# Kernel tuning notes

Hardware: AMD Instinct MI355X
Metric: run time of the kernel (lower is better)

The kernel has to match this reference:

```python
import jax, jax.numpy as jnp
import numpy as np

# Model dims (match init_kwargs)
B, L, DH = 4, 1024, 2048
D = 128          # head_dim
HQ, HK, HV = 16, 4, 4
H = 16           # expanded_num_heads = max(HQ, HK, HV)
K = 4            # short conv kernel size
EPS = 1e-5


def causal_depthwise_conv_silu(x, w):
    """ShortConvolution: causal depthwise conv1d + SiLU. x: [B,L,C], w: [C,K]."""
    Lx = x.shape[1]
    xp = jnp.pad(x, ((0, 0), (K - 1, 0), (0, 0)))
    y = sum(xp[:, j:j + Lx] * w[:, j] for j in range(K))
    return jax.nn.silu(y)


def _l2norm(t):
    return t * jax.lax.rsqrt(jnp.sum(t * t, axis=-1, keepdims=True) + 1e-6)


def setup_inputs() -> dict:
    key = jax.random.key(0)
    ks = jax.random.split(key, 14)
    s = 0.02
    # dt_bias init per module: dt ~ logspace(1e-3, 1e-1), inv softplus
    u = jax.random.uniform(ks[7], (H,))
    dt = jnp.exp(u * (np.log(0.1) - np.log(0.001)) + np.log(0.001))
    dt = jnp.clip(dt, 1e-4)
    dt_bias = dt + jnp.log(-jnp.expm1(-dt))
    return {
        "hidden_states": jax.random.normal(ks[0], (B, L, DH), jnp.float32),
        "Wq": jax.random.normal(ks[1], (DH, HQ * D), jnp.float32) * s,
        "Wk": jax.random.normal(ks[2], (DH, HK * D), jnp.float32) * s,
        "Wv": jax.random.normal(ks[3], (DH, HV * D), jnp.float32) * s,
        "Wb": jax.random.normal(ks[4], (DH, H), jnp.float32) * s,
        "Wgk": jax.random.normal(ks[5], (DH, H), jnp.float32) * s,
        "A_log": jnp.log(jax.random.uniform(ks[6], (H,), minval=1e-3, maxval=16.0)),
        "dt_bias": dt_bias,
        "conv_q": jax.random.normal(ks[8], (HQ * D, K), jnp.float32) * 0.1,
        "conv_k": jax.random.normal(ks[9], (HK * D, K), jnp.float32) * 0.1,
        "conv_v": jax.random.normal(ks[10], (HV * D, K), jnp.float32) * 0.1,
        "Wg": jax.random.normal(ks[11], (DH, H * D), jnp.float32) * s,
        "o_norm_w": jnp.ones((D,), jnp.float32),
        "Wo": jax.random.normal(ks[12], (H * D, DH), jnp.float32) * s,
    }


def reference(hidden_states, Wq, Wk, Wv, Wb, Wgk, A_log, dt_bias,
              conv_q, conv_k, conv_v, Wg, o_norm_w, Wo):
    x = hidden_states                                   # [B,L,DH]
    # projections + short causal conv + silu
    q = causal_depthwise_conv_silu(x @ Wq, conv_q).reshape(B, L, HQ, D)
    k = causal_depthwise_conv_silu(x @ Wk, conv_k).reshape(B, L, HK, D)
    v = causal_depthwise_conv_silu(x @ Wv, conv_v).reshape(B, L, HV, D)
    # GQA expansion: '... h d -> ... (h g) d' == repeat each head g times
    k = jnp.repeat(k, H // HK, axis=2)                  # [B,L,H,D]
    v = jnp.repeat(v, H // HV, axis=2)
    # gating scalars
    beta = jax.nn.sigmoid(x @ Wb)                       # [B,L,H]
    g = -jnp.exp(A_log) * jax.nn.softplus(x @ Wgk + dt_bias)  # [B,L,H] (log decay <= 0)
    # qk l2-norm (as in kernel), q scaled by D**-0.5
    q = _l2norm(q) * (D ** -0.5)
    k = _l2norm(k)
    # gated delta-rule recurrence: S_t = exp(g_t) S_{t-1} + beta_t k_t (v_t - k_t^T exp(g_t) S_{t-1})
    qT = q.transpose(1, 0, 2, 3)                        # [L,B,H,D]
    kT = k.transpose(1, 0, 2, 3)
    vT = v.transpose(1, 0, 2, 3)
    gT = g.transpose(1, 0, 2)                           # [L,B,H]
    bT = beta.transpose(1, 0, 2)

    def step(S, inp):
        q_t, k_t, v_t, g_t, b_t = inp
        S = S * jnp.exp(g_t)[..., None, None]           # decay state [B,H,D,D]
        v_res = v_t - jnp.einsum('bhk,bhkv->bhv', k_t, S)
        S = S + b_t[..., None, None] * (k_t[..., None] * v_res[:, :, None, :])
        o_t = jnp.einsum('bhk,bhkv->bhv', q_t, S)
        return S, o_t

    S0 = jnp.zeros((B, H, D, D), jnp.float32)
    _, oT = jax.lax.scan(step, S0, (qT, kT, vT, gT, bT))
    o = oT.transpose(1, 0, 2, 3)                        # [B,L,H,D]
    # FusedRMSNormGated: rmsnorm(o) * w * silu(gate), then output projection
    gate = (x @ Wg).reshape(B, L, H, D)
    o = o * jax.lax.rsqrt(jnp.mean(o * o, axis=-1, keepdims=True) + EPS)
    o = o * o_norm_w * jax.nn.silu(gate)
    return o.reshape(B, L, H * D) @ Wo                  # [B,L,DH]
```

## Files before the change

kernel.cpp:

```cpp
#include <hip/hip_runtime.h>
#include <hip/hip_bf16.h>
#include <math.h>

#define Bb 4
#define Ls 1024
#define DHc 2048
#define Dh 128
#define HQc 16
#define HKc 4
#define Hc 16
#define Mrows 4096
#define CC 64
#define NCH 16

typedef __attribute__((ext_vector_type(8))) short bf16x8;
typedef __attribute__((ext_vector_type(4))) float f32x4;

__device__ inline unsigned short f2b(float f) {
    __hip_bfloat16 h = __float2bfloat16(f);
    return *(unsigned short*)&h;
}
__device__ inline float b2f(unsigned short u) {
    __hip_bfloat16 h = *(__hip_bfloat16*)&u;
    return __bfloat162float(h);
}
__device__ inline bf16x8 scale_frag(bf16x8 a, float s) {
    union { bf16x8 v; unsigned short u[8]; } x;
    x.v = a;
#pragma unroll
    for (int i = 0; i < 8; i++) x.u[i] = f2b(b2f(x.u[i]) * s);
    return x.v;
}

__device__ inline void load_lds16(const void* g, void* l) {
    __builtin_amdgcn_global_load_lds((const __attribute__((address_space(1))) void*)g,
                                     (__attribute__((address_space(3))) void*)l, 16, 0, 0);
}

__device__ inline void bar_lds() {
    asm volatile("s_waitcnt lgkmcnt(0)" ::: "memory");
    __builtin_amdgcn_s_barrier();
    asm volatile("" ::: "memory");
}

__global__ void f32_to_bf16(const float* __restrict__ in, __hip_bfloat16* __restrict__ out, int n)
{
    int i = (blockIdx.x * 256 + threadIdx.x) * 4;
    if (i >= n) return;
    float4 v = *(const float4*)(in + i);
    __hip_bfloat16 h[4];
    h[0] = __float2bfloat16(v.x); h[1] = __float2bfloat16(v.y);
    h[2] = __float2bfloat16(v.z); h[3] = __float2bfloat16(v.w);
    *(uint2*)(out + i) = *(uint2*)h;
}

__launch_bounds__(256)
__global__ void transpose_to_bf16(const float* __restrict__ W, __hip_bfloat16* __restrict__ BT,
                                  int Krows, int Ncols)
{
    __shared__ float tile[64][65];
    const int n0 = blockIdx.x * 64, k0 = blockIdx.y * 64;
    const int tx = threadIdx.x & 63, ty = threadIdx.x >> 6;
#pragma unroll
    for (int r = ty; r < 64; r += 4)
        tile[r][tx] = W[(size_t)(k0 + r) * Ncols + n0 + tx];
    __syncthreads();
#pragma unroll
    for (int r = ty; r < 64; r += 4)
        BT[(size_t)(n0 + r) * Krows + k0 + tx] = __float2bfloat16(tile[tx][r]);
}

__launch_bounds__(256)
__global__ void gemm_bt_bf16(const __hip_bfloat16* __restrict__ A, const __hip_bfloat16* __restrict__ BT,
                             void* __restrict__ C, int N, int K, int c_bf16)
{
    __shared__ __align__(16) unsigned short As[128 * 32];
    __shared__ __align__(16) unsigned short Bs[128 * 32];
    const int tid = threadIdx.x;
    const int lane = tid & 63;
    const int wave = tid >> 6;
    const int wm = (wave >> 1) * 64, wn = (wave & 1) * 64;
    const int row0 = blockIdx.y * 128, col0 = blockIdx.x * 128;

    const int r0 = (wave * 2 + 0) * 16 + (lane >> 2);
    const int r1 = (wave * 2 + 1) * 16 + (lane >> 2);
    const int kk = ((lane & 3) ^ ((lane >> 3) & 3)) * 8;
    const __hip_bfloat16* Ap0 = A + (size_t)(row0 + r0) * K + kk;
    const __hip_bfloat16* Ap1 = A + (size_t)(row0 + r1) * K + kk;
    const __hip_bfloat16* Bp0 = BT + (size_t)(col0 + r0) * K + kk;
    const __hip_bfloat16* Bp1 = BT + (size_t)(col0 + r1) * K + kk;
    unsigned short* sa0 = &As[(wave * 2 + 0) * 16 * 32];
    unsigned short* sa1 = &As[(wave * 2 + 1) * 16 * 32];
    unsigned short* sb0 = &Bs[(wave * 2 + 0) * 16 * 32];
    unsigned short* sb1 = &Bs[(wave * 2 + 1) * 16 * 32];

    f32x4 acc[4][4];
#pragma unroll
    for (int i = 0; i < 4; i++)
#pragma unroll
        for (int j = 0; j < 4; j++) acc[i][j] = (f32x4){0.f, 0.f, 0.f, 0.f};

    const int fr = lane & 15;
    const int fs = (((lane >> 4) ^ ((fr >> 1) & 3))) * 8;

    for (int k0 = 0; k0 < K; k0 += 32) {
        __syncthreads();
        load_lds16(Ap0, sa0);
        load_lds16(Ap1, sa1);
        load_lds16(Bp0, sb0);
        load_lds16(Bp1, sb1);
        Ap0 += 32; Ap1 += 32; Bp0 += 32; Bp1 += 32;
        __syncthreads();

        bf16x8 af[4], bfr[4];
#pragma unroll
        for (int i = 0; i < 4; i++)
            af[i] = *(const bf16x8*)&As[(wm + i * 16 + fr) * 32 + fs];
#pragma unroll
        for (int j = 0; j < 4; j++)
            bfr[j] = *(const bf16x8*)&Bs[(wn + j * 16 + fr) * 32 + fs];
#pragma unroll
        for (int i = 0; i < 4; i++)
#pragma unroll
            for (int j = 0; j < 4; j++)
                acc[i][j] = __builtin_amdgcn_mfma_f32_16x16x32_bf16(af[i], bfr[j], acc[i][j], 0, 0, 0);
    }

    const int cr = (lane >> 4) * 4;
    const int cc = lane & 15;
#pragma unroll
    for (int i = 0; i < 4; i++)
#pragma unroll
        for (int j = 0; j < 4; j++) {
            size_t base = (size_t)(row0 + wm + i * 16 + cr) * N + (col0 + wn + j * 16 + cc);
#pragma unroll
            for (int p = 0; p < 4; p++) {
                if (c_bf16)
                    ((__hip_bfloat16*)C)[base + (size_t)p * N] = __float2bfloat16(acc[i][j][p]);
                else
                    ((float*)C)[base + (size_t)p * N] = acc[i][j][p];
            }
        }
}

__launch_bounds__(256)
__global__ void gemm_proj_fused(const __hip_bfloat16* __restrict__ A, const __hip_bfloat16* __restrict__ BT,
                                __hip_bfloat16* __restrict__ preQ, __hip_bfloat16* __restrict__ preK,
                                __hip_bfloat16* __restrict__ preV, __hip_bfloat16* __restrict__ gate)
{
    const int K = 2048;
    __shared__ __align__(16) unsigned short As[128 * 32];
    __shared__ __align__(16) unsigned short Bs[128 * 32];
    const int tid = threadIdx.x;
    const int lane = tid & 63;
    const int wave = tid >> 6;
    const int wm = (wave >> 1) * 64, wn = (wave & 1) * 64;
    const int row0 = blockIdx.y * 128;
    const int cb = blockIdx.x;
    const int col0 = cb * 128;

    __hip_bfloat16* Cb; int Nloc, c0loc;
    if (cb < 16)      { Cb = preQ; Nloc = 2048; c0loc = cb * 128; }
    else if (cb < 20) { Cb = preK; Nloc = 512;  c0loc = (cb - 16) * 128; }
    else if (cb < 24) { Cb = preV; Nloc = 512;  c0loc = (cb - 20) * 128; }
    else              { Cb = gate; Nloc = 2048; c0loc = (cb - 24) * 128; }

    const int r0 = (wave * 2 + 0) * 16 + (lane >> 2);
    const int r1 = (wave * 2 + 1) * 16 + (lane >> 2);
    const int kk = ((lane & 3) ^ ((lane >> 3) & 3)) * 8;
    const __hip_bfloat16* Ap0 = A + (size_t)(row0 + r0) * K + kk;
    const __hip_bfloat16* Ap1 = A + (size_t)(row0 + r1) * K + kk;
    const __hip_bfloat16* Bp0 = BT + (size_t)(col0 + r0) * K + kk;
    const __hip_bfloat16* Bp1 = BT + (size_t)(col0 + r1) * K + kk;
    unsigned short* sa0 = &As[(wave * 2 + 0) * 16 * 32];
    unsigned short* sa1 = &As[(wave * 2 + 1) * 16 * 32];
    unsigned short* sb0 = &Bs[(wave * 2 + 0) * 16 * 32];
    unsigned short* sb1 = &Bs[(wave * 2 + 1) * 16 * 32];

    f32x4 acc[4][4];
#pragma unroll
    for (int i = 0; i < 4; i++)
#pragma unroll
        for (int j = 0; j < 4; j++) acc[i][j] = (f32x4){0.f, 0.f, 0.f, 0.f};

    const int fr = lane & 15;
    const int fs = (((lane >> 4) ^ ((fr >> 1) & 3))) * 8;

    for (int k0 = 0; k0 < K; k0 += 32) {
        __syncthreads();
        load_lds16(Ap0, sa0);
        load_lds16(Ap1, sa1);
        load_lds16(Bp0, sb0);
        load_lds16(Bp1, sb1);
        Ap0 += 32; Ap1 += 32; Bp0 += 32; Bp1 += 32;
        __syncthreads();

        bf16x8 af[4], bfr[4];
#pragma unroll
        for (int i = 0; i < 4; i++)
            af[i] = *(const bf16x8*)&As[(wm + i * 16 + fr) * 32 + fs];
#pragma unroll
        for (int j = 0; j < 4; j++)
            bfr[j] = *(const bf16x8*)&Bs[(wn + j * 16 + fr) * 32 + fs];
#pragma unroll
        for (int i = 0; i < 4; i++)
#pragma unroll
            for (int j = 0; j < 4; j++)
                acc[i][j] = __builtin_amdgcn_mfma_f32_16x16x32_bf16(af[i], bfr[j], acc[i][j], 0, 0, 0);
    }

    const int cr = (lane >> 4) * 4;
    const int cc = lane & 15;
#pragma unroll
    for (int i = 0; i < 4; i++)
#pragma unroll
        for (int j = 0; j < 4; j++) {
            size_t base = (size_t)(row0 + wm + i * 16 + cr) * Nloc + (c0loc + wn + j * 16 + cc);
#pragma unroll
            for (int p = 0; p < 4; p++)
                Cb[base + (size_t)p * Nloc] = __float2bfloat16(acc[i][j][p]);
        }
}

__global__ void conv_silu_norm(const __hip_bfloat16* __restrict__ pre, const float* __restrict__ w,
                               __hip_bfloat16* __restrict__ out, int NH, int do_norm, float scale)
{
    __shared__ float red[2];
    const int idx = blockIdx.x;
    const int head = idx % NH;
    const int l = (idx / NH) % Ls;
    const int b = idx / (NH * Ls);
    const int C = NH * Dh;
    const int c = head * Dh + threadIdx.x;
    const __hip_bfloat16* base = pre + ((size_t)b * Ls + l) * C + c;
    const float4 wv = *(const float4*)(w + (size_t)c * 4);

    float v0 = (l >= 3) ? __bfloat162float(base[-3 * C]) : 0.f;
    float v1 = (l >= 2) ? __bfloat162float(base[-2 * C]) : 0.f;
    float v2 = (l >= 1) ? __bfloat162float(base[-1 * C]) : 0.f;
    float v3 = __bfloat162float(base[0]);
    float y = v0 * wv.x + v1 * wv.y + v2 * wv.z + v3 * wv.w;
    y = y / (1.f + expf(-y));

    if (do_norm) {
        float ss = y * y;
#pragma unroll
        for (int off = 32; off > 0; off >>= 1) ss += __shfl_xor(ss, off);
        if ((threadIdx.x & 63) == 0) red[threadIdx.x >> 6] = ss;
        __syncthreads();
        float tot = red[0] + red[1];
        y = y * rsqrtf(tot + 1e-6f) * scale;
    }
    out[((size_t)b * Ls + l) * C + c] = __float2bfloat16(y);
}

__global__ void pack_wt32(const float* __restrict__ Wb, const float* __restrict__ Wgk,
                          __hip_bfloat16* __restrict__ WT)
{
    const int t = blockIdx.x * 64 + (threadIdx.x & 63);
    const int h0 = (threadIdx.x >> 6) * 4;
#pragma unroll
    for (int i = 0; i < 4; i++) {
        const int h = h0 + i;
        WT[(size_t)h * 2048 + t]        = __float2bfloat16(Wb[(size_t)t * 16 + h]);
        WT[(size_t)(16 + h) * 2048 + t] = __float2bfloat16(Wgk[(size_t)t * 16 + h]);
    }
}

__launch_bounds__(256)
__global__ void proj_bg(const __hip_bfloat16* __restrict__ xbf, const __hip_bfloat16* __restrict__ WT32,
                        const float* __restrict__ A_log, const float* __restrict__ dt_bias,
                        float* __restrict__ beta, float* __restrict__ g)
{
    const int tid = threadIdx.x;
    const int lane = tid & 63;
    const int wave = tid >> 6;
    const int q = lane >> 4;
    const int cL = lane & 15;
    const int row0 = blockIdx.x * 64 + wave * 16;

    const unsigned short* xu = (const unsigned short*)xbf;
    const unsigned short* wu = (const unsigned short*)WT32;

    f32x4 accB = (f32x4){0.f, 0.f, 0.f, 0.f};
    f32x4 accG = (f32x4){0.f, 0.f, 0.f, 0.f};
    const size_t arow = (size_t)(row0 + cL) * 2048;
    const size_t brow = (size_t)cL * 2048;
    const size_t grow = (size_t)(16 + cL) * 2048;

#pragma unroll 4
    for (int k = 0; k < 2048; k += 32) {
        bf16x8 af  = *(const bf16x8*)&xu[arow + k + q * 8];
        bf16x8 wbf = *(const bf16x8*)&wu[brow + k + q * 8];
        bf16x8 wgf = *(const bf16x8*)&wu[grow + k + q * 8];
        accB = __builtin_amdgcn_mfma_f32_16x16x32_bf16(af, wbf, accB, 0, 0, 0);
        accG = __builtin_amdgcn_mfma_f32_16x16x32_bf16(af, wgf, accG, 0, 0, 0);
    }

    const float al = __expf(A_log[cL]);
    const float db = dt_bias[cL];
#pragma unroll
    for (int p = 0; p < 4; p++) {
        const int r = row0 + 4 * q + p;
        beta[(size_t)r * 16 + cL] = 1.f / (1.f + __expf(-accB[p]));
        float z = accG[p] + db;
        float sp = (z > 20.f) ? z : log1pf(__expf(z));
        g[(size_t)r * 16 + cL] = -al * sp;
    }
}

__global__ void bcum_kernel(const float* __restrict__ g, float* __restrict__ bcum)
{
    const int c = blockIdx.x & 15;
    const int bh = blockIdx.x >> 4;
    const int b = bh >> 4;
    const int h = bh & 15;
    const int t = threadIdx.x;
    float v = g[((size_t)(b * Ls + c * CC + t)) * 16 + h];
#pragma unroll
    for (int d = 1; d < 64; d <<= 1) {
        float n = __shfl_up(v, d, 64);
        if (t >= d) v += n;
    }
    bcum[(size_t)blockIdx.x * 64 + t] = v;
}

__launch_bounds__(256)
__global__ void gdn_phase1(const __hip_bfloat16* __restrict__ kc, const __hip_bfloat16* __restrict__ vc,
                           const float* __restrict__ bb, const float* __restrict__ bcum,
                           __hip_bfloat16* __restrict__ U, __hip_bfloat16* __restrict__ Z)
{
    const int task = blockIdx.x;
    const int c = task & 15;
    const int bh = task >> 4;
    const int b = bh >> 4;
    const int h = bh & 15;
    const int hk = h >> 2;
    const int tid = threadIdx.x;
    const int lane = tid & 63;
    const int wave = tid >> 6;
    const int q = lane >> 4;
    const int cL = lane & 15;

    __shared__ float Ab[64][68];
    __shared__ float sbeta[64], sbc[64];

    if (tid < 64) {
        sbeta[tid] = bb[((size_t)(b * Ls + c * CC + tid)) * 16 + h];
        sbc[tid] = bcum[((size_t)bh * 16 + c) * 64 + tid];
    }
    __syncthreads();

    const unsigned short* ku = (const unsigned short*)kc;
    const unsigned short* vu = (const unsigned short*)vc;

    f32x4 pacc[4];
#pragma unroll
    for (int j = 0; j < 4; j++) pacc[j] = (f32x4){0.f, 0.f, 0.f, 0.f};
    {
        const int t = 16 * wave + cL;
        const size_t krow = (((size_t)(b * Ls + c * CC + t)) * 4 + hk) * 128;
#pragma unroll
        for (int ks = 0; ks < 4; ks++) {
            bf16x8 af = *(const bf16x8*)&ku[krow + ks * 32 + q * 8];
#pragma unroll
            for (int j = 0; j < 4; j++) {
                const int s = 16 * j + cL;
                bf16x8 bf = *(const bf16x8*)&ku[(((size_t)(b * Ls + c * CC + s)) * 4 + hk) * 128 + ks * 32 + q * 8];
                pacc[j] = __builtin_amdgcn_mfma_f32_16x16x32_bf16(af, bf, pacc[j], 0, 0, 0);
            }
        }
    }
#pragma unroll
    for (int j = 0; j < 4; j++)
#pragma unroll
        for (int p = 0; p < 4; p++) {
            const int t = 16 * wave + 4 * q + p;
            const int s = 16 * j + cL;
            float val = 0.f;
            if (s < t) val = sbeta[t] * __expf(sbc[t] - sbc[s]) * pacc[j][p];
            Ab[t][s] = val;
        }
    __syncthreads();

    float u[64];
    const int j = tid;
    if (j < 128) {
#pragma unroll
        for (int t = 0; t < 64; t++)
            u[t] = sbeta[t] * b2f(vu[(((size_t)(b * Ls + c * CC + t)) * 4 + hk) * 128 + j]);
    } else {
        const int k = j - 128;
#pragma unroll
        for (int t = 0; t < 64; t++)
            u[t] = sbeta[t] * __expf(sbc[t]) * b2f(ku[(((size_t)(b * Ls + c * CC + t)) * 4 + hk) * 128 + k]);
    }
#pragma unroll
    for (int t = 1; t < 64; t++) {
        const float4* ar = (const float4*)Ab[t];
        const int nf = (t + 3) >> 2;
        float a0 = 0.f, a1 = 0.f, a2 = 0.f, a3 = 0.f;
#pragma unroll
        for (int i = 0; i < nf; i++) {
            float4 av = ar[i];
            a0 = fmaf(av.x, u[4 * i + 0], a0);
            a1 = fmaf(av.y, u[4 * i + 1], a1);
            a2 = fmaf(av.z, u[4 * i + 2], a2);
            a3 = fmaf(av.w, u[4 * i + 3], a3);
        }
        u[t] -= (a0 + a1) + (a2 + a3);
    }
    const size_t slab = ((size_t)bh * 16 + c) * 8192;
    if (j < 128) {
        unsigned short* Up = (unsigned short*)U + slab + (size_t)j * 64;
#pragma unroll
        for (int t8 = 0; t8 < 8; t8++) {
            union { bf16x8 v; unsigned short us[8]; } pk;
#pragma unroll
            for (int e = 0; e < 8; e++) pk.us[e] = f2b(u[8 * t8 + e]);
            *(bf16x8*)&Up[t8 * 8] = pk.v;
        }
    } else {
#pragma unroll
        for (int t = 0; t < 64; t++) Z[slab + t * 128 + (j - 128)] = __float2bfloat16(u[t]);
    }
}

__launch_bounds__(256, 1)
__global__ void gdn_phase2(const __hip_bfloat16* __restrict__ qc, const __hip_bfloat16* __restrict__ kc,
                           __hip_bfloat16* Uw ,
                           const __hip_bfloat16* __restrict__ Zbuf,
                           const float* __restrict__ bcum, float* __restrict__ Obuf)
{
    const int blk = blockIdx.x;
    const int quarter = blk & 3;
    const int bh = blk >> 2;
    const int b = bh >> 4;
    const int h = bh & 15;
    const int hk = h >> 2;
    const int vbase = quarter * 32;
    const int tid = threadIdx.x;
    const int lane = tid & 63;
    const int wave = tid >> 6;
    const int q = lane >> 4;
    const int cL = lane & 15;

    __shared__ __align__(16) unsigned short Tb[32 * 136];
    __shared__ __align__(16) unsigned short Kt[128 * 72];
    __shared__ __align__(16) unsigned short Wt[32 * 72];
    __shared__ __align__(16) unsigned short Us[32 * 72];

    const unsigned short* qu = (const unsigned short*)qc;
    const unsigned short* ku = (const unsigned short*)kc;
    unsigned short* Uu = (unsigned short*)Uw;
    const unsigned short* Zu = (const unsigned short*)Zbuf;

    const int tloc = tid & 63;
    const int kg = tid >> 6;
    const int trow = 16 * wave + cL;
    const int wv = (wave & 1) * 16;
    const int wk = (wave >> 1) * 4;

    f32x4 Tacc[4];
#pragma unroll
    for (int j = 0; j < 4; j++) Tacc[j] = (f32x4){0.f, 0.f, 0.f, 0.f};

    bf16x8 Kreg[4], Zreg[4], Qreg[4];
    uint4 Ureg;
    float p_bctl, p_bc63;
    float4 p_bct4;

    auto prefetch = [&](int c) {
        const size_t base_t = (size_t)b * Ls + (size_t)c * CC;
        const size_t slab = ((size_t)bh * 16 + c) * 8192;
        const size_t krow = ((base_t + tloc) * 4 + hk) * 128 + 32 * kg;
#pragma unroll
        for (int m = 0; m < 4; m++) Kreg[m] = *(const bf16x8*)&ku[krow + m * 8];
        Ureg = *(const uint4*)&Uu[slab + (size_t)(vbase + (tid >> 3)) * 64 + (tid & 7) * 8];
        const size_t zrow = slab + (size_t)trow * 128;
        const size_t qrow = ((base_t + trow) * 16 + h) * 128;
#pragma unroll
        for (int ks = 0; ks < 4; ks++) {
            Zreg[ks] = *(const bf16x8*)&Zu[zrow + ks * 32 + q * 8];
            Qreg[ks] = *(const bf16x8*)&qu[qrow + ks * 32 + q * 8];
        }
        const float* bc = bcum + ((size_t)bh * 16 + c) * 64;
        p_bctl = bc[tloc];
        p_bc63 = bc[63];
        p_bct4 = *(const float4*)&bc[16 * wave + 4 * q];
    };

    prefetch(0);

    for (int c = 0; c < NCH; ++c) {
        bf16x8 kr[4], zr[4], qr[4];
        uint4 ur;
#pragma unroll
        for (int m = 0; m < 4; m++) { kr[m] = Kreg[m]; zr[m] = Zreg[m]; qr[m] = Qreg[m]; }
        ur = Ureg;
        const float bctl = p_bctl, bc63 = p_bc63;
        const float4 bct4 = p_bct4;
        const size_t slab = ((size_t)bh * 16 + c) * 8192;

        if (c + 1 < NCH) prefetch(c + 1);

        const float ek = __expf(bc63 - bctl);
        const float eC = __expf(bc63);

        bar_lds();

#pragma unroll
        for (int m = 0; m < 4; m++) {
            union { bf16x8 v; unsigned short us[8]; } kv;
            kv.v = scale_frag(kr[m], ek);
#pragma unroll
            for (int e = 0; e < 8; e++) Kt[(32 * kg + 8 * m + e) * 72 + tloc] = kv.us[e];
        }
        *(uint4*)&Us[(tid >> 3) * 72 + (tid & 7) * 8] = ur;
#pragma unroll
        for (int j = 0; j < 4; j++)
#pragma unroll
            for (int p = 0; p < 4; p++)
                Tb[(wv + 4 * q + p) * 136 + (wave >> 1) * 64 + 16 * j + cL] = f2b(Tacc[j][p]);

        bar_lds();

        f32x4 Wacc[2], Oacc[2];
#pragma unroll
        for (int j = 0; j < 2; j++) { Wacc[j] = (f32x4){0.f,0.f,0.f,0.f}; Oacc[j] = (f32x4){0.f,0.f,0.f,0.f}; }
#pragma unroll
        for (int ks = 0; ks < 4; ks++) {
#pragma unroll
            for (int j = 0; j < 2; j++) {
                bf16x8 bt = *(const bf16x8*)&Tb[(16 * j + cL) * 136 + 32 * ks + 8 * q];
                Wacc[j] = __builtin_amdgcn_mfma_f32_16x16x32_bf16(zr[ks], bt, Wacc[j], 0, 0, 0);
                Oacc[j] = __builtin_amdgcn_mfma_f32_16x16x32_bf16(qr[ks], bt, Oacc[j], 0, 0, 0);
            }
        }
        float e4[4] = {__expf(bct4.x), __expf(bct4.y), __expf(bct4.z), __expf(bct4.w)};
#pragma unroll
        for (int j = 0; j < 2; j++)
#pragma unroll
            for (int p = 0; p < 4; p++) {
                const int t = 16 * wave + 4 * q + p;
                const int v = 16 * j + cL;
                const float w = b2f(Us[v * 72 + t]) - Wacc[j][p];
                Wt[v * 72 + t] = f2b(w);
                Obuf[((size_t)b * Ls + c * CC + t) * 2048 + h * 128 + vbase + v] = Oacc[j][p] * e4[p];
            }

        bar_lds();

        {
            const int vloc = tid >> 3, part = tid & 7;
            const size_t dst = slab + (size_t)(vbase + vloc) * 64 + part * 8;
            *(uint4*)&Uu[dst] = *(const uint4*)&Wt[vloc * 72 + part * 8];
        }
#pragma unroll
        for (int j = 0; j < 4; j++)
#pragma unroll
            for (int p = 0; p < 4; p++) Tacc[j][p] *= eC;
#pragma unroll
        for (int ks = 0; ks < 2; ks++) {
            bf16x8 aw = *(const bf16x8*)&Wt[(wv + cL) * 72 + 32 * ks + 8 * q];
#pragma unroll
            for (int j = 0; j < 4; j++) {
                bf16x8 bk = *(const bf16x8*)&Kt[((wk + j) * 16 + cL) * 72 + 32 * ks + 8 * q];
                Tacc[j] = __builtin_amdgcn_mfma_f32_16x16x32_bf16(aw, bk, Tacc[j], 0, 0, 0);
            }
        }
    }
}

__launch_bounds__(256)
__global__ void gdn_phase3(const __hip_bfloat16* __restrict__ qc, const __hip_bfloat16* __restrict__ kc,
                           const __hip_bfloat16* __restrict__ WT, const float* __restrict__ bcum,
                           float* __restrict__ Obuf)
{
    const int task = blockIdx.x;
    const int c = task & 15;
    const int bh = task >> 4;
    const int b = bh >> 4;
    const int h = bh & 15;
    const int hk = h >> 2;
    const int tid = threadIdx.x;
    const int lane = tid & 63;
    const int wave = tid >> 6;
    const int q = lane >> 4;
    const int cL = lane & 15;

    __shared__ __align__(16) unsigned short Mb[64 * 72];
    __shared__ float sbc[64];

    if (tid < 64) sbc[tid] = bcum[((size_t)bh * 16 + c) * 64 + tid];
    __syncthreads();

    const unsigned short* qu = (const unsigned short*)qc;
    const unsigned short* ku = (const unsigned short*)kc;
    const unsigned short* wu = (const unsigned short*)WT;

    f32x4 pacc[4];
#pragma unroll
    for (int j = 0; j < 4; j++) pacc[j] = (f32x4){0.f, 0.f, 0.f, 0.f};
    {
        const int t = 16 * wave + cL;
        const size_t qrow = (((size_t)(b * Ls + c * CC + t)) * 16 + h) * 128;
#pragma unroll
        for (int ks = 0; ks < 4; ks++) {
            bf16x8 aq = *(const bf16x8*)&qu[qrow + ks * 32 + q * 8];
#pragma unroll
            for (int j = 0; j < 4; j++) {
                const int s = 16 * j + cL;
                bf16x8 bk = *(const bf16x8*)&ku[(((size_t)(b * Ls + c * CC + s)) * 4 + hk) * 128 + ks * 32 + q * 8];
                pacc[j] = __builtin_amdgcn_mfma_f32_16x16x32_bf16(aq, bk, pacc[j], 0, 0, 0);
            }
        }
    }
#pragma unroll
    for (int j = 0; j < 4; j++)
#pragma unroll
        for (int p = 0; p < 4; p++) {
            const int t = 16 * wave + 4 * q + p;
            const int s = 16 * j + cL;
            const float val = (s <= t) ? __expf(sbc[t] - sbc[s]) * pacc[j][p] : 0.f;
            Mb[t * 72 + s] = f2b(val);
        }
    __syncthreads();

    f32x4 oacc[8];
#pragma unroll
    for (int j = 0; j < 8; j++) oacc[j] = (f32x4){0.f, 0.f, 0.f, 0.f};
    const size_t slab = ((size_t)bh * 16 + c) * 8192;
#pragma unroll
    for (int ks = 0; ks < 2; ks++) {
        bf16x8 am = *(const bf16x8*)&Mb[(16 * wave + cL) * 72 + ks * 32 + q * 8];
#pragma unroll
        for (int j = 0; j < 8; j++) {
            const int v = 16 * j + cL;
            bf16x8 bw = *(const bf16x8*)&wu[slab + (size_t)v * 64 + ks * 32 + q * 8];
            oacc[j] = __builtin_amdgcn_mfma_f32_16x16x32_bf16(am, bw, oacc[j], 0, 0, 0);
        }
    }
#pragma unroll
    for (int j = 0; j < 8; j++)
#pragma unroll
        for (int p = 0; p < 4; p++) {
            const int t = 16 * wave + 4 * q + p;
            const int v = 16 * j + cL;
            const size_t a = ((size_t)(b * Ls + c * CC + t)) * 2048 + h * 128 + v;
            Obuf[a] += oacc[j][p];
        }
}

__global__ void gated_rmsnorm(const float* __restrict__ o, const __hip_bfloat16* __restrict__ gate,
                              const float* __restrict__ w, __hip_bfloat16* __restrict__ out)
{
    const size_t row = blockIdx.x;
    const float* op = o + row * Dh;
    const __hip_bfloat16* gp = gate + row * Dh;
    const int t = threadIdx.x;
    float o0 = op[t], o1 = op[t + 64];
    float ss = o0 * o0 + o1 * o1;
#pragma unroll
    for (int off = 32; off > 0; off >>= 1) ss += __shfl_xor(ss, off);
    float r = rsqrtf(ss * (1.f / 128.f) + 1e-5f);
    float g0 = __bfloat162float(gp[t]), g1 = __bfloat162float(gp[t + 64]);
    out[row * Dh + t]      = __float2bfloat16(o0 * r * w[t]      * (g0 / (1.f + expf(-g0))));
    out[row * Dh + t + 64] = __float2bfloat16(o1 * r * w[t + 64] * (g1 / (1.f + expf(-g1))));
}

extern "C" void kernel_launch(void* const* d_in, const int* in_sizes, int n_in,
                              void* d_out, int out_size, void* d_ws, size_t ws_size,
                              hipStream_t stream)
{
    const float* x     = (const float*)d_in[0];
    const float* Wq    = (const float*)d_in[1];
    const float* Wk    = (const float*)d_in[2];
    const float* Wv    = (const float*)d_in[3];
    const float* Wb    = (const float*)d_in[4];
    const float* Wgk   = (const float*)d_in[5];
    const float* A_log = (const float*)d_in[6];
    const float* dtb   = (const float*)d_in[7];
    const float* cq    = (const float*)d_in[8];
    const float* ck    = (const float*)d_in[9];
    const float* cv    = (const float*)d_in[10];
    const float* Wg    = (const float*)d_in[11];
    const float* onw   = (const float*)d_in[12];
    const float* Wo    = (const float*)d_in[13];

    char* wsb = (char*)d_ws;
    __hip_bfloat16* xbf  = (__hip_bfloat16*)(wsb + 0);
    __hip_bfloat16* qcb  = (__hip_bfloat16*)(wsb + 16777216);
    __hip_bfloat16* kcb  = (__hip_bfloat16*)(wsb + 33554432);
    __hip_bfloat16* vcb  = (__hip_bfloat16*)(wsb + 37748736);
    __hip_bfloat16* Uw   = (__hip_bfloat16*)(wsb + 41943040);
    __hip_bfloat16* Zb   = (__hip_bfloat16*)(wsb + 58720256);
    float*          bcum = (float*)(wsb + 75497472);

    __hip_bfloat16* Zdelta = xbf;

    __hip_bfloat16* BTall = qcb;

    char* dob = (char*)d_out;
    __hip_bfloat16* preQ = (__hip_bfloat16*)dob;
    __hip_bfloat16* preK = (__hip_bfloat16*)(dob + 16777216);
    __hip_bfloat16* preV = (__hip_bfloat16*)(dob + 20971520);
    float* bb = (float*)(dob + 25165824);
    float* gb = (float*)(dob + 25427968);
    __hip_bfloat16* WT32 = (__hip_bfloat16*)(dob + 25690112);
    float* Obuf = (float*)d_out;

    const float qscale = 0.08838834764831845f;
    const int nx = Mrows * DHc;

    f32_to_bf16<<<nx / 4 / 256, 256, 0, stream>>>(x, xbf, nx);
    pack_wt32<<<32, 256, 0, stream>>>(Wb, Wgk, WT32);
    proj_bg<<<64, 256, 0, stream>>>(xbf, WT32, A_log, dtb, bb, gb);
    bcum_kernel<<<64 * NCH, 64, 0, stream>>>(gb, bcum);

    transpose_to_bf16<<<dim3(32, 32), 256, 0, stream>>>(Wq, BTall, 2048, 2048);
    transpose_to_bf16<<<dim3(8, 32), 256, 0, stream>>>(Wk, BTall + (size_t)2048 * 2048, 2048, 512);
    transpose_to_bf16<<<dim3(8, 32), 256, 0, stream>>>(Wv, BTall + (size_t)2560 * 2048, 2048, 512);
    transpose_to_bf16<<<dim3(32, 32), 256, 0, stream>>>(Wg, BTall + (size_t)3072 * 2048, 2048, 2048);

    gemm_proj_fused<<<dim3(40, 32), 256, 0, stream>>>(xbf, BTall, preQ, preK, preV, Zb);

    conv_silu_norm<<<Mrows * HQc, 128, 0, stream>>>(preQ, cq, qcb, HQc, 1, qscale);
    conv_silu_norm<<<Mrows * HKc, 128, 0, stream>>>(preK, ck, kcb, HKc, 1, 1.0f);
    conv_silu_norm<<<Mrows * HKc, 128, 0, stream>>>(preV, cv, vcb, HKc, 0, 1.0f);

    gdn_phase1<<<64 * NCH, 256, 0, stream>>>(kcb, vcb, bb, bcum, Uw, Zdelta);
    gdn_phase2<<<256, 256, 0, stream>>>(qcb, kcb, Uw, Zdelta, bcum, Obuf);
    gdn_phase3<<<64 * NCH, 256, 0, stream>>>(qcb, kcb, Uw, bcum, Obuf);

    gated_rmsnorm<<<Mrows * Hc, 64, 0, stream>>>(Obuf, Zb, onw, qcb);
    transpose_to_bf16<<<dim3(32, 32), 256, 0, stream>>>(Wo, (__hip_bfloat16*)Uw, 2048, 2048);
    gemm_bt_bf16<<<dim3(16, 32), 256, 0, stream>>>(qcb, (__hip_bfloat16*)Uw, d_out, 2048, 2048, 0);
}
```

Baseline: 540.1 us.

## Fuse gated RMSNorm into phase3, merge weight transposes, narrow output GEMM tile

Gated RMSNorm now runs in the gdn_phase3 epilogue. Each block adds its intra-chunk output to the Obuf partial, reduces the sum of squares across 16 lanes with shuffles, applies the silu gate, and writes bf16 directly. This removes the fp32 Obuf read-modify-write pass and a separate 65536-block kernel. The four weight-transpose launches are merged into one kernel. The output GEMM uses a 128x64 tile, giving 1024 blocks instead of 512 to better fill the CUs, at the cost of less B-tile reuse.

New measurement: 507.6 us. 6.0% less time.

```diff
diff --git a/kernel.cpp b/kernel.cpp
--- a/kernel.cpp
+++ b/kernel.cpp
@@ -71,34 +71,57 @@
 }
 
 __launch_bounds__(256)
-__global__ void gemm_bt_bf16(const __hip_bfloat16* __restrict__ A, const __hip_bfloat16* __restrict__ BT,
-                             void* __restrict__ C, int N, int K, int c_bf16)
+__global__ void transpose_all_bf16(const float* __restrict__ Wq, const float* __restrict__ Wk,
+                                   const float* __restrict__ Wv, const float* __restrict__ Wg,
+                                   __hip_bfloat16* __restrict__ BTall)
+{
+    const int lb = blockIdx.x;
+    const float* W; __hip_bfloat16* BT; int Ncols, bx, by;
+    if (lb < 1024)      { W = Wq; BT = BTall;                          Ncols = 2048; int r = lb;        bx = r & 31; by = r >> 5; }
+    else if (lb < 1280) { W = Wk; BT = BTall + (size_t)2048 * 2048;    Ncols = 512;  int r = lb - 1024; bx = r & 7;  by = r >> 3; }
+    else if (lb < 1536) { W = Wv; BT = BTall + (size_t)2560 * 2048;    Ncols = 512;  int r = lb - 1280; bx = r & 7;  by = r >> 3; }
+    else                { W = Wg; BT = BTall + (size_t)3072 * 2048;    Ncols = 2048; int r = lb - 1536; bx = r & 31; by = r >> 5; }
+
+    __shared__ float tile[64][65];
+    const int n0 = bx * 64, k0 = by * 64;
+    const int tx = threadIdx.x & 63, ty = threadIdx.x >> 6;
+#pragma unroll
+    for (int r = ty; r < 64; r += 4)
+        tile[r][tx] = W[(size_t)(k0 + r) * Ncols + n0 + tx];
+    __syncthreads();
+#pragma unroll
+    for (int r = ty; r < 64; r += 4)
+        BT[(size_t)(n0 + r) * 2048 + k0 + tx] = __float2bfloat16(tile[tx][r]);
+}
+
+__launch_bounds__(256)
+__global__ void gemm_bt_n64_f32(const __hip_bfloat16* __restrict__ A, const __hip_bfloat16* __restrict__ BT,
+                                float* __restrict__ C, int N, int K)
 {
     __shared__ __align__(16) unsigned short As[128 * 32];
-    __shared__ __align__(16) unsigned short Bs[128 * 32];
+    __shared__ __align__(16) unsigned short Bs[64 * 32];
     const int tid = threadIdx.x;
     const int lane = tid & 63;
     const int wave = tid >> 6;
-    const int wm = (wave >> 1) * 64, wn = (wave & 1) * 64;
-    const int row0 = blockIdx.y * 128, col0 = blockIdx.x * 128;
-
-    const int r0 = (wave * 2 + 0) * 16 + (lane >> 2);
-    const int r1 = (wave * 2 + 1) * 16 + (lane >> 2);
+    const int wm = (wave >> 1) * 64, wn = (wave & 1) * 32;
+    const int row0 = blockIdx.y * 128, col0 = blockIdx.x * 64;
+
+    const int rA0 = wave * 16 + (lane >> 2);
+    const int rA1 = 64 + wave * 16 + (lane >> 2);
+    const int rB  = wave * 16 + (lane >> 2);
     const int kk = ((lane & 3) ^ ((lane >> 3) & 3)) * 8;
-    const __hip_bfloat16* Ap0 = A + (size_t)(row0 + r0) * K + kk;
-    const __hip_bfloat16* Ap1 = A + (size_t)(row0 + r1) * K + kk;
-    const __hip_bfloat16* Bp0 = BT + (size_t)(col0 + r0) * K + kk;
-    const __hip_bfloat16* Bp1 = BT + (size_t)(col0 + r1) * K + kk;
-    unsigned short* sa0 = &As[(wave * 2 + 0) * 16 * 32];
-    unsigned short* sa1 = &As[(wave * 2 + 1) * 16 * 32];
-    unsigned short* sb0 = &Bs[(wave * 2 + 0) * 16 * 32];
-    unsigned short* sb1 = &Bs[(wave * 2 + 1) * 16 * 32];
-
-    f32x4 acc[4][4];
+    const __hip_bfloat16* Ap0 = A + (size_t)(row0 + rA0) * K + kk;
+    const __hip_bfloat16* Ap1 = A + (size_t)(row0 + rA1) * K + kk;
+    const __hip_bfloat16* Bp0 = BT + (size_t)(col0 + rB) * K + kk;
+    unsigned short* sa0 = &As[(wave * 16) * 32];
+    unsigned short* sa1 = &As[(64 + wave * 16) * 32];
+    unsigned short* sb0 = &Bs[(wave * 16) * 32];
+
+    f32x4 acc[4][2];
 #pragma unroll
     for (int i = 0; i < 4; i++)
 #pragma unroll
-        for (int j = 0; j < 4; j++) acc[i][j] = (f32x4){0.f, 0.f, 0.f, 0.f};
+        for (int j = 0; j < 2; j++) acc[i][j] = (f32x4){0.f, 0.f, 0.f, 0.f};
 
     const int fr = lane & 15;
     const int fs = (((lane >> 4) ^ ((fr >> 1) & 3))) * 8;
@@ -108,21 +131,20 @@
         load_lds16(Ap0, sa0);
         load_lds16(Ap1, sa1);
         load_lds16(Bp0, sb0);
-        load_lds16(Bp1, sb1);
-        Ap0 += 32; Ap1 += 32; Bp0 += 32; Bp1 += 32;
+        Ap0 += 32; Ap1 += 32; Bp0 += 32;
         __syncthreads();
 
-        bf16x8 af[4], bfr[4];
+        bf16x8 af[4], bfr[2];
 #pragma unroll
         for (int i = 0; i < 4; i++)
             af[i] = *(const bf16x8*)&As[(wm + i * 16 + fr) * 32 + fs];
 #pragma unroll
-        for (int j = 0; j < 4; j++)
+        for (int j = 0; j < 2; j++)
             bfr[j] = *(const bf16x8*)&Bs[(wn + j * 16 + fr) * 32 + fs];
 #pragma unroll
         for (int i = 0; i < 4; i++)
 #pragma unroll
-            for (int j = 0; j < 4; j++)
+            for (int j = 0; j < 2; j++)
                 acc[i][j] = __builtin_amdgcn_mfma_f32_16x16x32_bf16(af[i], bfr[j], acc[i][j], 0, 0, 0);
     }
 
@@ -131,15 +153,11 @@
 #pragma unroll
     for (int i = 0; i < 4; i++)
 #pragma unroll
-        for (int j = 0; j < 4; j++) {
+        for (int j = 0; j < 2; j++) {
             size_t base = (size_t)(row0 + wm + i * 16 + cr) * N + (col0 + wn + j * 16 + cc);
 #pragma unroll
-            for (int p = 0; p < 4; p++) {
-                if (c_bf16)
-                    ((__hip_bfloat16*)C)[base + (size_t)p * N] = __float2bfloat16(acc[i][j][p]);
-                else
-                    ((float*)C)[base + (size_t)p * N] = acc[i][j][p];
-            }
+            for (int p = 0; p < 4; p++)
+                C[base + (size_t)p * N] = acc[i][j][p];
         }
 }
 
@@ -575,7 +593,8 @@
 __launch_bounds__(256)
 __global__ void gdn_phase3(const __hip_bfloat16* __restrict__ qc, const __hip_bfloat16* __restrict__ kc,
                            const __hip_bfloat16* __restrict__ WT, const float* __restrict__ bcum,
-                           float* __restrict__ Obuf)
+                           const float* __restrict__ Obuf, const __hip_bfloat16* __restrict__ gate,
+                           const float* __restrict__ onw, __hip_bfloat16* __restrict__ nrm)
 {
     const int task = blockIdx.x;
     const int c = task & 15;
@@ -598,6 +617,8 @@
     const unsigned short* qu = (const unsigned short*)qc;
     const unsigned short* ku = (const unsigned short*)kc;
     const unsigned short* wu = (const unsigned short*)WT;
+    const unsigned short* gu = (const unsigned short*)gate;
+    unsigned short* nu = (unsigned short*)nrm;
 
     f32x4 pacc[4];
 #pragma unroll
@@ -641,32 +662,31 @@
             oacc[j] = __builtin_amdgcn_mfma_f32_16x16x32_bf16(am, bw, oacc[j], 0, 0, 0);
         }
     }
-#pragma unroll
-    for (int j = 0; j < 8; j++)
-#pragma unroll
-        for (int p = 0; p < 4; p++) {
-            const int t = 16 * wave + 4 * q + p;
+
+#pragma unroll
+    for (int p = 0; p < 4; p++) {
+        const int t = 16 * wave + 4 * q + p;
+        const size_t l = (size_t)(b * Ls + c * CC + t);
+        const size_t orow = l * 2048 + (size_t)h * 128;
+        const size_t xrow = (l * 16 + h) * 128;
+        float ov[8];
+        float ss = 0.f;
+#pragma unroll
+        for (int j = 0; j < 8; j++) {
             const int v = 16 * j + cL;
-            const size_t a = ((size_t)(b * Ls + c * CC + t)) * 2048 + h * 128 + v;
-            Obuf[a] += oacc[j][p];
-        }
-}
-
-__global__ void gated_rmsnorm(const float* __restrict__ o, const __hip_bfloat16* __restrict__ gate,
-                              const float* __restrict__ w, __hip_bfloat16* __restrict__ out)
-{
-    const size_t row = blockIdx.x;
-    const float* op = o + row * Dh;
-    const __hip_bfloat16* gp = gate + row * Dh;
-    const int t = threadIdx.x;
-    float o0 = op[t], o1 = op[t + 64];
-    float ss = o0 * o0 + o1 * o1;
-#pragma unroll
-    for (int off = 32; off > 0; off >>= 1) ss += __shfl_xor(ss, off);
-    float r = rsqrtf(ss * (1.f / 128.f) + 1e-5f);
-    float g0 = __bfloat162float(gp[t]), g1 = __bfloat162float(gp[t + 64]);
-    out[row * Dh + t]      = __float2bfloat16(o0 * r * w[t]      * (g0 / (1.f + expf(-g0))));
-    out[row * Dh + t + 64] = __float2bfloat16(o1 * r * w[t + 64] * (g1 / (1.f + expf(-g1))));
+            ov[j] = Obuf[orow + v] + oacc[j][p];
+            ss += ov[j] * ov[j];
+        }
+#pragma unroll
+        for (int m = 1; m < 16; m <<= 1) ss += __shfl_xor(ss, m);
+        const float r = rsqrtf(ss * (1.f / 128.f) + 1e-5f);
+#pragma unroll
+        for (int j = 0; j < 8; j++) {
+            const int v = 16 * j + cL;
+            const float gv = b2f(gu[xrow + v]);
+            nu[xrow + v] = f2b(ov[j] * r * onw[v] * (gv / (1.f + __expf(-gv))));
+        }
+    }
 }
 
 extern "C" void kernel_launch(void* const* d_in, const int* in_sizes, int n_in,
@@ -698,6 +718,7 @@
     float*          bcum = (float*)(wsb + 75497472);
 
     __hip_bfloat16* Zdelta = xbf;
+    __hip_bfloat16* nrm    = xbf;
 
     __hip_bfloat16* BTall = qcb;
 
@@ -718,10 +739,7 @@
     proj_bg<<<64, 256, 0, stream>>>(xbf, WT32, A_log, dtb, bb, gb);
     bcum_kernel<<<64 * NCH, 64, 0, stream>>>(gb, bcum);
 
-    transpose_to_bf16<<<dim3(32, 32), 256, 0, stream>>>(Wq, BTall, 2048, 2048);
-    transpose_to_bf16<<<dim3(8, 32), 256, 0, stream>>>(Wk, BTall + (size_t)2048 * 2048, 2048, 512);
-    transpose_to_bf16<<<dim3(8, 32), 256, 0, stream>>>(Wv, BTall + (size_t)2560 * 2048, 2048, 512);
-    transpose_to_bf16<<<dim3(32, 32), 256, 0, stream>>>(Wg, BTall + (size_t)3072 * 2048, 2048, 2048);
+    transpose_all_bf16<<<2560, 256, 0, stream>>>(Wq, Wk, Wv, Wg, BTall);
 
     gemm_proj_fused<<<dim3(40, 32), 256, 0, stream>>>(xbf, BTall, preQ, preK, preV, Zb);
 
@@ -731,9 +749,8 @@
 
     gdn_phase1<<<64 * NCH, 256, 0, stream>>>(kcb, vcb, bb, bcum, Uw, Zdelta);
     gdn_phase2<<<256, 256, 0, stream>>>(qcb, kcb, Uw, Zdelta, bcum, Obuf);
-    gdn_phase3<<<64 * NCH, 256, 0, stream>>>(qcb, kcb, Uw, bcum, Obuf);
-
-    gated_rmsnorm<<<Mrows * Hc, 64, 0, stream>>>(Obuf, Zb, onw, qcb);
+    gdn_phase3<<<64 * NCH, 256, 0, stream>>>(qcb, kcb, Uw, bcum, Obuf, Zb, onw, nrm);
+
     transpose_to_bf16<<<dim3(32, 32), 256, 0, stream>>>(Wo, (__hip_bfloat16*)Uw, 2048, 2048);
-    gemm_bt_bf16<<<dim3(16, 32), 256, 0, stream>>>(qcb, (__hip_bfloat16*)Uw, d_out, 2048, 2048, 0);
-}
+    gemm_bt_n64_f32<<<dim3(32, 32), 256, 0, stream>>>(nrm, (__hip_bfloat16*)Uw, (float*)d_out, 2048, 2048);
+}
```
